# Kernel optimization log

Measured on AMD Instinct MI355X. Metric: run time of the kernel, lower is better.

The kernel has to match this reference:

```python
import jax, jax.numpy as jnp
import numpy as np

N_EMBD = 256
BLOCK_SIZE = 128
N_HEAD = 8
HEAD_SIZE = 256
B = 256
T = 128


def setup_inputs() -> dict:
    key = jax.random.key(0)
    ks = jax.random.split(key, 9)
    s = 0.02
    return {
        "x": jax.random.normal(ks[0], (B, T, N_EMBD), dtype=jnp.float32),
        # torch Linear weight layout: [out_features, in_features], stacked over heads
        "Wq": jax.random.normal(ks[1], (N_HEAD, HEAD_SIZE, N_EMBD), dtype=jnp.float32) * s,
        "bq": jax.random.normal(ks[2], (N_HEAD, HEAD_SIZE), dtype=jnp.float32) * s,
        "Wk": jax.random.normal(ks[3], (N_HEAD, HEAD_SIZE, N_EMBD), dtype=jnp.float32) * s,
        "bk": jax.random.normal(ks[4], (N_HEAD, HEAD_SIZE), dtype=jnp.float32) * s,
        "Wv": jax.random.normal(ks[5], (N_HEAD, HEAD_SIZE, N_EMBD), dtype=jnp.float32) * s,
        "bv": jax.random.normal(ks[6], (N_HEAD, HEAD_SIZE), dtype=jnp.float32) * s,
        "Wp": jax.random.normal(ks[7], (N_EMBD, N_EMBD), dtype=jnp.float32) * s,
        "bp": jax.random.normal(ks[8], (N_EMBD,), dtype=jnp.float32) * s,
    }


def reference(x, Wq, bq, Wk, bk, Wv, bv, Wp, bp):
    Bb, Tt, C = x.shape
    scale = C ** (-0.5)  # NOTE: original scales by n_embd (input C), not head_size
    # per-head projections: [h, b, t, d]
    q = jnp.einsum("btc,hdc->hbtd", x, Wq) + bq[:, None, None, :]
    k = jnp.einsum("btc,hdc->hbtd", x, Wk) + bk[:, None, None, :]
    v = jnp.einsum("btc,hdc->hbtd", x, Wv) + bv[:, None, None, :]
    att = jnp.einsum("hbtd,hbsd->hbts", q, k) * scale  # [h,b,t,s]
    causal = jnp.tril(jnp.ones((Tt, Tt), dtype=bool))
    att = jnp.where(causal, att, -jnp.inf)
    att = jax.nn.softmax(att, axis=-1)
    out = jnp.einsum("hbts,hbsd->hbtd", att, v)
    # torch.cat along dim=0 (batch concat, as written in the source)
    out = out.reshape(out.shape[0] * Bb, Tt, out.shape[-1])  # [h*b, t, head_size]
    return out @ Wp.T + bp
```

## Files before the change

kernel.cpp:

```cpp
#include <hip/hip_runtime.h>
#include <hip/hip_bf16.h>
#include <stdint.h>


#define TT 128

typedef __attribute__((ext_vector_type(8))) short short8;
typedef __attribute__((ext_vector_type(4))) float f32x4;

#define WS_X    0u
#define WS_M    16777216u
#define WS_WM   17825792u
#define WS_WB   18874368u
#define WS_BB   18939904u
#define WS_CQ   18948096u

#define LX     0
#define LT     65536
#define LP     65536
#define LH     98304
#define R_UV   131072
#define R_RED  132096
#define LDS_SIZE 134144

#define VMCNT0() asm volatile("s_waitcnt vmcnt(0)" ::: "memory")
#define LGKM0()  asm volatile("s_waitcnt lgkmcnt(0)" ::: "memory")
#define BAR()    do { asm volatile("" ::: "memory"); __builtin_amdgcn_s_barrier(); asm volatile("" ::: "memory"); } while (0)
#define PRIO1()  __builtin_amdgcn_s_setprio(1)
#define PRIO0()  __builtin_amdgcn_s_setprio(0)

typedef __attribute__((address_space(3))) uint32_t lds_u32;
typedef __attribute__((address_space(1))) const uint32_t glb_u32;

__device__ __forceinline__ unsigned short f2bf(float x) {
    union { float f; unsigned u; } v; v.f = x;
    unsigned r = v.u + 0x7FFFu + ((v.u >> 16) & 1u);
    return (unsigned short)(r >> 16);
}
__device__ __forceinline__ unsigned pk2(float a, float b) {
    return (unsigned)f2bf(a) | ((unsigned)f2bf(b) << 16);
}

__global__ __launch_bounds__(256) void convert_pre(
    const float* __restrict__ x,
    const float* __restrict__ Wq, const float* __restrict__ bq,
    const float* __restrict__ Wk, const float* __restrict__ bk,
    const float* __restrict__ Wv, const float* __restrict__ bv,
    const float* __restrict__ Wp, const float* __restrict__ bp,
    char* __restrict__ ws)
{
    extern __shared__ char clds[];
    const int tid = threadIdx.x;
    const int bid = blockIdx.x;

    if (bid < 256) {
        const float* src = x + (size_t)bid * 32768;
        char* dst = ws + WS_X + (size_t)bid * 65536;
        for (int i = tid; i < 8192; i += 256) {
            float4 v = ((const float4*)src)[i];
            int row = i >> 6, c4 = i & 63;
            uint2 u; u.x = pk2(v.x, v.y); u.y = pk2(v.z, v.w);
            *(uint2*)(clds + row * 512 + ((c4 * 8) ^ ((row & 7) << 4))) = u;
        }
        __syncthreads();
        for (int i = tid; i < 4096; i += 256) {
            int l = i & 63, ks = (i >> 6) & 7, g = i >> 9;
            int r = g * 16 + (l & 15);
            int boff = ks * 64 + (l >> 4) * 16;
            uint4 q = *(const uint4*)(clds + r * 512 + (boff ^ ((r & 7) << 4)));
            ((uint4*)dst)[i] = q;
        }
        return;
    }
    if (bid < 384) {
        int id = bid - 256, h = id >> 4, st = id & 15;
        float* wkL = (float*)clds;
        for (int i = tid; i < 4096; i += 256) {
            int d = i >> 4, cc = i & 15;
            wkL[i] = Wk[(size_t)h * 65536 + d * 256 + st * 16 + cc];
        }
        __syncthreads();
        const int c = tid;
        float acc[16];
        #pragma unroll
        for (int j = 0; j < 16; ++j) acc[j] = 0.f;
        #pragma unroll 4
        for (int d = 0; d < 256; ++d) {
            float a = Wq[(size_t)h * 65536 + d * 256 + c];
            #pragma unroll
            for (int j = 0; j < 16; ++j) acc[j] += a * wkL[d * 16 + j];
        }
        char* base = ws + WS_M + (size_t)h * 131072;
        int ks = c >> 5, lgp = (c >> 3) & 3, jb = c & 7;
        #pragma unroll
        for (int j = 0; j < 16; ++j) {
            int cp = st * 16 + j;
            *(unsigned short*)(base + (((st * 8 + ks)) << 10)
                + ((cp & 15) + 16 * lgp) * 16 + jb * 2) = f2bf(acc[j] * 0.0625f);
        }
        return;
    }
    if (bid < 512) {
        int id = bid - 384, h = id >> 4, st = id & 15;
        float* wpL = (float*)clds;
        for (int i = tid; i < 4096; i += 256) {
            int e = i >> 8, d = i & 255;
            wpL[e * 257 + d] = Wp[(size_t)(st * 16 + e) * 256 + d];
        }
        __syncthreads();
        const int c = tid;
        float acc[16];
        #pragma unroll
        for (int j = 0; j < 16; ++j) acc[j] = 0.f;
        #pragma unroll 4
        for (int d = 0; d < 256; ++d) {
            float wv = Wv[(size_t)h * 65536 + d * 256 + c];
            #pragma unroll
            for (int j = 0; j < 16; ++j) acc[j] += wv * wpL[j * 257 + d];
        }
        char* base = ws + WS_WM + (size_t)h * 131072;
        int ks = c >> 5, lgp = (c >> 3) & 3, jb = c & 7;
        #pragma unroll
        for (int j = 0; j < 16; ++j) {
            *(unsigned short*)(base + (((st * 8 + ks)) << 10)
                + (j + 16 * lgp) * 16 + jb * 2) = f2bf(acc[j]);
        }
        return;
    }
    if (bid < 520) {
        const int h = bid - 512;
        {
            uint4 z = {0u,0u,0u,0u};
            for (int i = tid; i < 512; i += 256)
                ((uint4*)(ws + WS_WB + (size_t)h * 8192))[i] = z;
        }
        float* tK = (float*)clds;
        float* tQ = (float*)(clds + 16384);
        const int c = tid;
        float s1 = 0.f, s2 = 0.f;
        for (int d0 = 0; d0 < 256; d0 += 16) {
            __syncthreads();
            for (int i = tid; i < 1024; i += 256) {
                int row = i >> 6, c4 = i & 63;
                ((float4*)tK)[row * 64 + c4] =
                    ((const float4*)(Wk + (size_t)h * 65536 + (size_t)(d0 + row) * 256))[c4];
                ((float4*)tQ)[row * 64 + c4] =
                    ((const float4*)(Wq + (size_t)h * 65536 + (size_t)(d0 + row) * 256))[c4];
            }
            __syncthreads();
            #pragma unroll
            for (int dd = 0; dd < 16; ++dd) {
                s1 += tK[dd * 256 + c] * bq[h * 256 + d0 + dd];
                s2 += tQ[dd * 256 + c] * bk[h * 256 + d0 + dd];
            }
        }
        int ks = c >> 5, lgp = (c >> 3) & 3, jb = c & 7;
        char* base = ws + WS_WB + (size_t)h * 8192 + ks * 1024;
        *(unsigned short*)(base + (0 + 16 * lgp) * 16 + jb * 2) = f2bf(s2 * 0.0625f);
        *(unsigned short*)(base + (1 + 16 * lgp) * 16 + jb * 2) = f2bf(s1 * 0.0625f);
        float* red = (float*)(clds + 32768);
        red[tid] = bq[h * 256 + tid] * bk[h * 256 + tid];
        __syncthreads();
        if (tid == 0) {
            float cq = 0.f;
            for (int d = 0; d < 256; ++d) cq += red[d];
            *(float*)(ws + WS_CQ + h * 4) = cq * 0.0625f;
        }
        return;
    }
    {
        const int st = bid - 520;
        float* wpT = (float*)clds;
        float* bvL = (float*)(clds + 17408);
        for (int i = tid; i < 1024; i += 256) {
            int row = i >> 6, c4 = i & 63;
            float4 v = ((const float4*)(Wp + (size_t)(st * 16 + row) * 256))[c4];
            float* dstp = wpT + row * 257 + c4 * 4;
            dstp[0] = v.x; dstp[1] = v.y; dstp[2] = v.z; dstp[3] = v.w;
        }
        for (int i = tid; i < 512; i += 256)
            ((float4*)bvL)[i] = ((const float4*)bv)[i];
        __syncthreads();
        const int el = tid >> 4, dg = tid & 15;
        #pragma unroll
        for (int h = 0; h < 8; ++h) {
            float p = 0.f;
            #pragma unroll
            for (int dd = 0; dd < 16; ++dd) {
                int d = dg * 16 + dd;
                p += bvL[h * 256 + d] * wpT[el * 257 + d];
            }
            p += __shfl_xor(p, 1);
            p += __shfl_xor(p, 2);
            p += __shfl_xor(p, 4);
            p += __shfl_xor(p, 8);
            if (dg == 0)
                *(float*)(ws + WS_BB + (size_t)h * 1024 + (st * 16 + el) * 4)
                    = bp[st * 16 + el] + p;
        }
        return;
    }
}

__global__ __launch_bounds__(1024, 1) void mha_fused(
    const char* __restrict__ ws, float* __restrict__ out)
{
    extern __shared__ char lds[];
    const int tid = threadIdx.x;
    const int w  = tid >> 6, l = tid & 63;
    const int lg = l >> 4, lr = l & 15;
    const int mq = w & 7, nh = w >> 3;
    const int bid = blockIdx.x;
    const int xcd = bid & 7, j = bid >> 3;
    const int h = j & 7;
    const int b = ((j >> 3) << 3) | xcd;
    const size_t orow = ((size_t)(h * 256 + b)) * TT;

    const char* Xf  = ws + WS_X  + (size_t)b * 65536;
    const char* Mh  = ws + WS_M  + (size_t)h * 131072;
    const char* WMh = ws + WS_WM + (size_t)h * 131072;
    const char* WBh = ws + WS_WB + (size_t)h * 8192;

    {
        const char* src = Xf + tid * 16;
        #pragma unroll
        for (int p = 0; p < 4; ++p)
            __builtin_amdgcn_global_load_lds((glb_u32*)(src + p * 16384),
                (lds_u32*)(lds + LX + tid * 16 + p * 16384), 16, 0, 0);
    }
    VMCNT0(); BAR();

    if (nh == 0) {
        f32x4 vacc = f32x4{0.f,0.f,0.f,0.f};
        #pragma unroll
        for (int ks = 0; ks < 8; ++ks) {
            short8 wb = *(const short8*)(WBh + (ks << 10) + l*16);
            short8 xa = *(const short8*)(lds + LX + (((mq*8 + ks)) << 10) + l*16);
            vacc = __builtin_amdgcn_mfma_f32_16x16x32_bf16(xa, wb, vacc, 0, 0, 0);
        }
        if (lr < 2) {
            #pragma unroll
            for (int r = 0; r < 4; ++r) {
                int t = mq*16 + lg*4 + r;
                *(float*)(lds + R_UV + lr*512 + t*4) = vacc[r];
            }
        }
    }

    {
        f32x4 acc[8];
        #pragma unroll
        for (int i = 0; i < 8; ++i) acc[i] = f32x4{0.f,0.f,0.f,0.f};
        #pragma unroll
        for (int ks = 0; ks < 8; ++ks) {
            short8 nb = *(const short8*)(Mh + (((w*8 + ks)) << 10) + l*16);
            PRIO1();
            #pragma unroll
            for (int mt = 0; mt < 8; ++mt) {
                short8 xa = *(const short8*)(lds + LX + (((mt*8 + ks)) << 10) + l*16);
                acc[mt] = __builtin_amdgcn_mfma_f32_16x16x32_bf16(xa, nb, acc[mt], 0, 0, 0);
            }
            PRIO0();
        }
        #pragma unroll
        for (int mt = 0; mt < 8; ++mt)
            #pragma unroll
            for (int r = 0; r < 4; ++r) {
                int t = mt*16 + lg*4 + r;
                int c = w*16 + lr;
                *(unsigned short*)(lds + LT + t*512 + ((c*2) ^ ((t&7)<<4)))
                    = f2bf(acc[mt][r]);
            }
    }
    LGKM0(); BAR();

    f32x4 sacc[4];
    #pragma unroll
    for (int i = 0; i < 4; ++i) sacc[i] = f32x4{0.f,0.f,0.f,0.f};
    #pragma unroll
    for (int ks2 = 0; ks2 < 8; ++ks2) {
        int t2 = mq*16 + lr;
        short8 ta = *(const short8*)(lds + LT + t2*512 + ((ks2*64 + lg*16) ^ ((t2&7)<<4)));
        short8 sb[4];
        #pragma unroll
        for (int nt = 0; nt < 4; ++nt)
            sb[nt] = *(const short8*)(lds + LX + (((nh*4+nt)*8 + ks2) << 10) + l*16);
        PRIO1();
        #pragma unroll
        for (int nt = 0; nt < 4; ++nt)
            sacc[nt] = __builtin_amdgcn_mfma_f32_16x16x32_bf16(ta, sb[nt], sacc[nt], 0, 0, 0);
        PRIO0();
    }

    {
        const float cq = *(const float*)(ws + WS_CQ + h*4);
        float uu[4];
        #pragma unroll
        for (int nt = 0; nt < 4; ++nt)
            uu[nt] = *(const float*)(lds + R_UV + 512 + (nh*64 + nt*16 + lr)*4);
        float* redM = (float*)(lds + R_RED);
        float* redS = redM + 256;
        float rmax[4];
        #pragma unroll
        for (int r = 0; r < 4; ++r) {
            int t = mq*16 + lg*4 + r;
            float vt = *(const float*)(lds + R_UV + t*4) + cq;
            float m = -1e30f;
            #pragma unroll
            for (int nt = 0; nt < 4; ++nt) {
                int s = nh*64 + nt*16 + lr;
                float sv = sacc[nt][r] + vt + uu[nt];
                if (s > t) sv = -1e30f;
                sacc[nt][r] = sv;
                m = fmaxf(m, sv);
            }
            m = fmaxf(m, __shfl_xor(m, 1));
            m = fmaxf(m, __shfl_xor(m, 2));
            m = fmaxf(m, __shfl_xor(m, 4));
            m = fmaxf(m, __shfl_xor(m, 8));
            rmax[r] = m;
        }
        if (lr == 0) {
            #pragma unroll
            for (int r = 0; r < 4; ++r)
                redM[nh*128 + mq*16 + lg*4 + r] = rmax[r];
        }
        LGKM0(); BAR();
        float rsum[4];
        #pragma unroll
        for (int r = 0; r < 4; ++r) {
            int t = mq*16 + lg*4 + r;
            float m = fmaxf(redM[t], redM[128 + t]);
            float ssum = 0.f;
            #pragma unroll
            for (int nt = 0; nt < 4; ++nt) {
                float p = __expf(sacc[nt][r] - m);
                sacc[nt][r] = p;
                ssum += p;
            }
            ssum += __shfl_xor(ssum, 1);
            ssum += __shfl_xor(ssum, 2);
            ssum += __shfl_xor(ssum, 4);
            ssum += __shfl_xor(ssum, 8);
            rsum[r] = ssum;
        }
        if (lr == 0) {
            #pragma unroll
            for (int r = 0; r < 4; ++r)
                redS[nh*128 + mq*16 + lg*4 + r] = rsum[r];
        }
        LGKM0(); BAR();
        #pragma unroll
        for (int r = 0; r < 4; ++r) {
            int t = mq*16 + lg*4 + r;
            float inv = 1.0f / (redS[t] + redS[128 + t]);
            #pragma unroll
            for (int nt = 0; nt < 4; ++nt) {
                int s = nh*64 + nt*16 + lr;
                *(unsigned short*)(lds + LP + t*256 + ((s*2) ^ ((t&7)<<4)))
                    = f2bf(sacc[nt][r] * inv);
            }
        }
    }
    LGKM0(); BAR();

    short8 pa[4];
    {
        int t2 = mq*16 + lr;
        #pragma unroll
        for (int ks = 0; ks < 4; ++ks)
            pa[ks] = *(const short8*)(lds + LP + t2*256 + ((ks*64 + lg*16) ^ ((t2&7)<<4)));
    }

    const float* bbp = (const float*)(ws + WS_BB + h*1024);
    #pragma unroll
    for (int eh = 0; eh < 2; ++eh) {
        {
            f32x4 acc[4];
            #pragma unroll
            for (int i = 0; i < 4; ++i) acc[i] = f32x4{0.f,0.f,0.f,0.f};
            #pragma unroll
            for (int ks = 0; ks < 8; ++ks) {
                short8 wa = *(const short8*)(WMh + ((((eh*8 + mq)*8 + ks)) << 10) + l*16);
                PRIO1();
                #pragma unroll
                for (int nt = 0; nt < 4; ++nt) {
                    short8 sb = *(const short8*)(lds + LX + ((((nh*4+nt)*8 + ks)) << 10) + l*16);
                    acc[nt] = __builtin_amdgcn_mfma_f32_16x16x32_bf16(wa, sb, acc[nt], 0, 0, 0);
                }
                PRIO0();
            }
            #pragma unroll
            for (int nt = 0; nt < 4; ++nt)
                #pragma unroll
                for (int r = 0; r < 4; ++r) {
                    int el = mq*16 + lg*4 + r;
                    int s  = (nh*4+nt)*16 + lr;
                    *(unsigned short*)(lds + LH + el*256 + ((s*2) ^ ((el&7)<<4)))
                        = f2bf(acc[nt][r]);
                }
        }
        LGKM0(); BAR();
        #pragma unroll
        for (int ec = 0; ec < 2; ++ec) {
            f32x4 acc[2];
            acc[0] = f32x4{0.f,0.f,0.f,0.f};
            acc[1] = f32x4{0.f,0.f,0.f,0.f};
            #pragma unroll
            for (int ks = 0; ks < 4; ++ks) {
                short8 hb[2];
                #pragma unroll
                for (int nt = 0; nt < 2; ++nt) {
                    int erl = nh*64 + (ec*2 + nt)*16 + lr;
                    hb[nt] = *(const short8*)(lds + LH + erl*256 + ((ks*64 + lg*16) ^ ((erl&7)<<4)));
                }
                PRIO1();
                #pragma unroll
                for (int nt = 0; nt < 2; ++nt)
                    acc[nt] = __builtin_amdgcn_mfma_f32_16x16x32_bf16(pa[ks], hb[nt], acc[nt], 0, 0, 0);
                PRIO0();
            }
            #pragma unroll
            for (int nt = 0; nt < 2; ++nt) {
                int e = eh*128 + nh*64 + (ec*2 + nt)*16 + lr;
                float bbv = bbp[e];
                #pragma unroll
                for (int r = 0; r < 4; ++r) {
                    int t = mq*16 + lg*4 + r;
                    out[(orow + t) * 256 + e] = acc[nt][r] + bbv;
                }
            }
        }
        if (eh == 0) { LGKM0(); BAR(); }
    }
}

extern "C" void kernel_launch(void* const* d_in, const int* in_sizes, int n_in,
                              void* d_out, int out_size, void* d_ws, size_t ws_size,
                              hipStream_t stream) {
    (void)in_sizes; (void)n_in; (void)out_size; (void)ws_size;
    const float* x  = (const float*)d_in[0];
    const float* Wq = (const float*)d_in[1];
    const float* bq = (const float*)d_in[2];
    const float* Wk = (const float*)d_in[3];
    const float* bk = (const float*)d_in[4];
    const float* Wv = (const float*)d_in[5];
    const float* bv = (const float*)d_in[6];
    const float* Wp = (const float*)d_in[7];
    const float* bp = (const float*)d_in[8];
    char* ws = (char*)d_ws;

    hipFuncSetAttribute((const void*)convert_pre,
                        hipFuncAttributeMaxDynamicSharedMemorySize, 65536);
    convert_pre<<<dim3(536), dim3(256), 65536, stream>>>(
        x, Wq, bq, Wk, bk, Wv, bv, Wp, bp, ws);

    hipFuncSetAttribute((const void*)mha_fused,
                        hipFuncAttributeMaxDynamicSharedMemorySize, LDS_SIZE);
    mha_fused<<<dim3(2048), dim3(1024), LDS_SIZE, stream>>>(ws, (float*)d_out);
}
```

Before: 239.0 us.

## Retile per-wave MFMA blocks to 2D tiles and vectorize weight-prep LDS reads

The main attention-stage GEMMs now give each wave a 2D register tile (4x2 or 2x2 MFMA blocks) instead of a 1D strip. Each loaded A/B fragment is reused across more MFMAs, which cuts redundant LDS and global fragment loads per MFMA. The weight-precompute blocks now read their staged operands as float4 from LDS, using a transposed padded layout for Wp. The 2D tiles raise register pressure and change the LDS access patterns.

Result: no change. 236.3 us (-1.1%).

```diff
diff --git a/kernel.cpp b/kernel.cpp
--- a/kernel.cpp
+++ b/kernel.cpp
@@ -81,15 +81,19 @@
         }
         __syncthreads();
         const int c = tid;
-        float acc[16];
-        #pragma unroll
-        for (int j = 0; j < 16; ++j) acc[j] = 0.f;
+        float4 a0 = {0,0,0,0}, a1 = {0,0,0,0}, a2 = {0,0,0,0}, a3 = {0,0,0,0};
+        const float4* wk4 = (const float4*)wkL;
         #pragma unroll 4
         for (int d = 0; d < 256; ++d) {
             float a = Wq[(size_t)h * 65536 + d * 256 + c];
-            #pragma unroll
-            for (int j = 0; j < 16; ++j) acc[j] += a * wkL[d * 16 + j];
-        }
+            float4 k0 = wk4[d*4+0], k1 = wk4[d*4+1], k2 = wk4[d*4+2], k3 = wk4[d*4+3];
+            a0.x += a*k0.x; a0.y += a*k0.y; a0.z += a*k0.z; a0.w += a*k0.w;
+            a1.x += a*k1.x; a1.y += a*k1.y; a1.z += a*k1.z; a1.w += a*k1.w;
+            a2.x += a*k2.x; a2.y += a*k2.y; a2.z += a*k2.z; a2.w += a*k2.w;
+            a3.x += a*k3.x; a3.y += a*k3.y; a3.z += a*k3.z; a3.w += a*k3.w;
+        }
+        float acc[16] = {a0.x,a0.y,a0.z,a0.w, a1.x,a1.y,a1.z,a1.w,
+                         a2.x,a2.y,a2.z,a2.w, a3.x,a3.y,a3.z,a3.w};
         char* base = ws + WS_M + (size_t)h * 131072;
         int ks = c >> 5, lgp = (c >> 3) & 3, jb = c & 7;
         #pragma unroll
@@ -102,22 +106,29 @@
     }
     if (bid < 512) {
         int id = bid - 384, h = id >> 4, st = id & 15;
-        float* wpL = (float*)clds;
-        for (int i = tid; i < 4096; i += 256) {
-            int e = i >> 8, d = i & 255;
-            wpL[e * 257 + d] = Wp[(size_t)(st * 16 + e) * 256 + d];
+        float* wpT2 = (float*)clds;
+        for (int i = tid; i < 1024; i += 256) {
+            int e = i >> 6, d4 = i & 63;
+            float4 v = ((const float4*)(Wp + (size_t)(st * 16 + e) * 256))[d4];
+            int d = d4 * 4;
+            wpT2[(d+0)*20+e] = v.x; wpT2[(d+1)*20+e] = v.y;
+            wpT2[(d+2)*20+e] = v.z; wpT2[(d+3)*20+e] = v.w;
         }
         __syncthreads();
         const int c = tid;
-        float acc[16];
-        #pragma unroll
-        for (int j = 0; j < 16; ++j) acc[j] = 0.f;
+        float4 a0 = {0,0,0,0}, a1 = {0,0,0,0}, a2 = {0,0,0,0}, a3 = {0,0,0,0};
         #pragma unroll 4
         for (int d = 0; d < 256; ++d) {
             float wv = Wv[(size_t)h * 65536 + d * 256 + c];
-            #pragma unroll
-            for (int j = 0; j < 16; ++j) acc[j] += wv * wpL[j * 257 + d];
-        }
+            const float4* wp4 = (const float4*)(wpT2 + d * 20);
+            float4 p0 = wp4[0], p1 = wp4[1], p2 = wp4[2], p3 = wp4[3];
+            a0.x += wv*p0.x; a0.y += wv*p0.y; a0.z += wv*p0.z; a0.w += wv*p0.w;
+            a1.x += wv*p1.x; a1.y += wv*p1.y; a1.z += wv*p1.z; a1.w += wv*p1.w;
+            a2.x += wv*p2.x; a2.y += wv*p2.y; a2.z += wv*p2.z; a2.w += wv*p2.w;
+            a3.x += wv*p3.x; a3.y += wv*p3.y; a3.z += wv*p3.z; a3.w += wv*p3.w;
+        }
+        float acc[16] = {a0.x,a0.y,a0.z,a0.w, a1.x,a1.y,a1.z,a1.w,
+                         a2.x,a2.y,a2.z,a2.w, a3.x,a3.y,a3.z,a3.w};
         char* base = ws + WS_WM + (size_t)h * 131072;
         int ks = c >> 5, lgp = (c >> 3) & 3, jb = c & 7;
         #pragma unroll
@@ -248,29 +259,41 @@
     }
 
     {
-        f32x4 acc[8];
-        #pragma unroll
-        for (int i = 0; i < 8; ++i) acc[i] = f32x4{0.f,0.f,0.f,0.f};
+        const int th = w >> 3, cp = w & 7;
+        f32x4 acc[4][2];
+        #pragma unroll
+        for (int i = 0; i < 4; ++i)
+            #pragma unroll
+            for (int c2 = 0; c2 < 2; ++c2) acc[i][c2] = f32x4{0.f,0.f,0.f,0.f};
         #pragma unroll
         for (int ks = 0; ks < 8; ++ks) {
-            short8 nb = *(const short8*)(Mh + (((w*8 + ks)) << 10) + l*16);
+            short8 nb[2];
+            #pragma unroll
+            for (int c2 = 0; c2 < 2; ++c2)
+                nb[c2] = *(const short8*)(Mh + ((((cp*2+c2)*8 + ks)) << 10) + l*16);
+            short8 xa[4];
+            #pragma unroll
+            for (int i = 0; i < 4; ++i)
+                xa[i] = *(const short8*)(lds + LX + ((((th*4+i)*8 + ks)) << 10) + l*16);
             PRIO1();
             #pragma unroll
-            for (int mt = 0; mt < 8; ++mt) {
-                short8 xa = *(const short8*)(lds + LX + (((mt*8 + ks)) << 10) + l*16);
-                acc[mt] = __builtin_amdgcn_mfma_f32_16x16x32_bf16(xa, nb, acc[mt], 0, 0, 0);
-            }
+            for (int i = 0; i < 4; ++i)
+                #pragma unroll
+                for (int c2 = 0; c2 < 2; ++c2)
+                    acc[i][c2] = __builtin_amdgcn_mfma_f32_16x16x32_bf16(xa[i], nb[c2], acc[i][c2], 0, 0, 0);
             PRIO0();
         }
         #pragma unroll
-        for (int mt = 0; mt < 8; ++mt)
-            #pragma unroll
-            for (int r = 0; r < 4; ++r) {
-                int t = mt*16 + lg*4 + r;
-                int c = w*16 + lr;
-                *(unsigned short*)(lds + LT + t*512 + ((c*2) ^ ((t&7)<<4)))
-                    = f2bf(acc[mt][r]);
-            }
+        for (int i = 0; i < 4; ++i)
+            #pragma unroll
+            for (int c2 = 0; c2 < 2; ++c2)
+                #pragma unroll
+                for (int r = 0; r < 4; ++r) {
+                    int t = (th*4+i)*16 + lg*4 + r;
+                    int c = (cp*2+c2)*16 + lr;
+                    *(unsigned short*)(lds + LT + t*512 + ((c*2) ^ ((t&7)<<4)))
+                        = f2bf(acc[i][c2][r]);
+                }
     }
     LGKM0(); BAR();
 
@@ -376,29 +399,41 @@
     #pragma unroll
     for (int eh = 0; eh < 2; ++eh) {
         {
-            f32x4 acc[4];
-            #pragma unroll
-            for (int i = 0; i < 4; ++i) acc[i] = f32x4{0.f,0.f,0.f,0.f};
+            const int ep = w & 3, sp = w >> 2;
+            f32x4 acc[2][2];
+            #pragma unroll
+            for (int i = 0; i < 2; ++i)
+                #pragma unroll
+                for (int c2 = 0; c2 < 2; ++c2) acc[i][c2] = f32x4{0.f,0.f,0.f,0.f};
             #pragma unroll
             for (int ks = 0; ks < 8; ++ks) {
-                short8 wa = *(const short8*)(WMh + ((((eh*8 + mq)*8 + ks)) << 10) + l*16);
+                short8 wa[2];
+                #pragma unroll
+                for (int i = 0; i < 2; ++i)
+                    wa[i] = *(const short8*)(WMh + ((((eh*8 + ep*2+i)*8 + ks)) << 10) + l*16);
+                short8 sb[2];
+                #pragma unroll
+                for (int c2 = 0; c2 < 2; ++c2)
+                    sb[c2] = *(const short8*)(lds + LX + ((((sp*2+c2)*8 + ks)) << 10) + l*16);
                 PRIO1();
                 #pragma unroll
-                for (int nt = 0; nt < 4; ++nt) {
-                    short8 sb = *(const short8*)(lds + LX + ((((nh*4+nt)*8 + ks)) << 10) + l*16);
-                    acc[nt] = __builtin_amdgcn_mfma_f32_16x16x32_bf16(wa, sb, acc[nt], 0, 0, 0);
-                }
+                for (int i = 0; i < 2; ++i)
+                    #pragma unroll
+                    for (int c2 = 0; c2 < 2; ++c2)
+                        acc[i][c2] = __builtin_amdgcn_mfma_f32_16x16x32_bf16(wa[i], sb[c2], acc[i][c2], 0, 0, 0);
                 PRIO0();
             }
             #pragma unroll
-            for (int nt = 0; nt < 4; ++nt)
-                #pragma unroll
-                for (int r = 0; r < 4; ++r) {
-                    int el = mq*16 + lg*4 + r;
-                    int s  = (nh*4+nt)*16 + lr;
-                    *(unsigned short*)(lds + LH + el*256 + ((s*2) ^ ((el&7)<<4)))
-                        = f2bf(acc[nt][r]);
-                }
+            for (int i = 0; i < 2; ++i)
+                #pragma unroll
+                for (int c2 = 0; c2 < 2; ++c2)
+                    #pragma unroll
+                    for (int r = 0; r < 4; ++r) {
+                        int el = (ep*2+i)*16 + lg*4 + r;
+                        int s  = (sp*2+c2)*16 + lr;
+                        *(unsigned short*)(lds + LH + el*256 + ((s*2) ^ ((el&7)<<4)))
+                            = f2bf(acc[i][c2][r]);
+                    }
         }
         LGKM0(); BAR();
         #pragma unroll
```
